# Performance work log

Measured on AMD Instinct MI355X. Metric: run time of the kernel, lower is better.

Reference implementation:

```python
import jax, jax.numpy as jnp
import numpy as np

N_VERTS = 100000
N_FACES = 200000
C = 512


def setup_inputs() -> dict:
    key = jax.random.key(0)
    ks = jax.random.split(key, 12)
    x = jax.random.normal(ks[0], (1, N_VERTS, C), dtype=jnp.float32) * 0.1
    verts = jax.random.normal(ks[1], (N_VERTS, 3), dtype=jnp.float32)
    faces = jax.random.randint(ks[2], (N_FACES, 3), 0, N_VERTS, dtype=jnp.int32)
    def lin(k, fan_in, fan_out):
        return jax.random.normal(k, (fan_in, fan_out), dtype=jnp.float32) / np.sqrt(fan_in)
    return {
        "x": x, "verts": verts, "faces": faces,
        "W1": lin(ks[3], C, C),    "b1": jnp.zeros((C,), jnp.float32),
        "W2": lin(ks[4], C, 512),  "b2": jnp.zeros((512,), jnp.float32),
        "W3": lin(ks[5], 512, 256),"b3": jnp.zeros((256,), jnp.float32),
        "W4": lin(ks[6], 256, 12), "b4": jnp.zeros((12,), jnp.float32),
    }


def special_procrustes(M):
    # roma.special_procrustes: nearest rotation in SO(3) to M, batched [F,3,3]
    U, S, Vh = jnp.linalg.svd(M)
    det = jnp.linalg.det(jnp.matmul(U, Vh))  # [F]
    D = jnp.stack([jnp.ones_like(det), jnp.ones_like(det), det], axis=-1)  # [F,3]
    return jnp.matmul(U * D[:, None, :], Vh)


def reference(x, verts, faces, W1, b1, W2, b2, W3, b3, W4, b4):
    N = verts.shape[0]
    F = faces.shape[0]
    # prism base: gather 3 vertex positions per face -> [F,3,3]
    prism_base = verts[faces]
    # gather features of the 3 face vertices and mean over them -> [F,C]
    feat = x[0][faces].mean(axis=1)
    # mlp_refine
    h = jax.nn.relu(feat @ W1 + b1)
    h = jax.nn.relu(h @ W2 + b2)
    h = jax.nn.relu(h @ W3 + b3)
    out = h @ W4 + b4  # [F,12]
    # batched 3x3 Procrustes rotation + translation
    rotations = special_procrustes(out[:, :9].reshape(F, 3, 3))
    translations = out[:, 9:]  # [F,3]
    transformed_prism = jnp.matmul(prism_base, rotations) + translations[:, None, :]  # [F,3,3]
    # scatter-add back to vertices with per-vertex face-count normalization
    flat_idx = faces.reshape(-1)  # [3F]
    summed = jax.ops.segment_sum(transformed_prism.reshape(-1, 3), flat_idx, num_segments=N)
    counts = jax.ops.segment_sum(jnp.ones((3 * F,), jnp.float32), flat_idx, num_segments=N)
    features = summed / jnp.clip(counts, 1.0)[:, None]  # [N,3]
    return features[None], transformed_prism, rotations
```

## Files before the change

### kernel.cpp

```cpp
#include <hip/hip_runtime.h>
#include <stdint.h>

typedef __attribute__((ext_vector_type(8))) short short8;
typedef __attribute__((ext_vector_type(4))) float f32x4;
typedef __attribute__((ext_vector_type(4))) unsigned short u16x4;

__device__ __forceinline__ unsigned short f2bf(float x) {
    union { float f; uint32_t u; } v; v.f = x;
    uint32_t u = v.u;
    uint32_t r = (u + 0x7FFFu + ((u >> 16) & 1u)) >> 16;
    return (unsigned short)r;
}
__device__ __forceinline__ float bf2f(unsigned short h) {
    union { uint32_t u; float f; } v; v.u = ((uint32_t)h) << 16;
    return v.f;
}

__device__ __forceinline__ void gld_lds16(const void* g, void* s) {
    __builtin_amdgcn_global_load_lds(
        (const __attribute__((address_space(1))) void*)(uintptr_t)g,
        (__attribute__((address_space(3))) void*)(uint32_t)(uintptr_t)s,
        16, 0, 0);
}

__device__ __forceinline__ f32x4 mfma16(short8 a, short8 b, f32x4 c) {
    return __builtin_amdgcn_mfma_f32_16x16x32_bf16(a, b, c, 0, 0, 0);
}

__global__ void zero_kernel(float* __restrict__ sums, float* __restrict__ counts, int nverts) {
    int t = blockIdx.x * 256 + threadIdx.x;
    if (t < nverts * 3) sums[t] = 0.0f;
    if (t < nverts)     counts[t] = 0.0f;
}

__global__ void prep_weights(const float* __restrict__ W1, const float* __restrict__ W2,
                             const float* __restrict__ W3,
                             unsigned short* __restrict__ w1h, unsigned short* __restrict__ w1l,
                             unsigned short* __restrict__ w2h, unsigned short* __restrict__ w2l,
                             unsigned short* __restrict__ w3h, unsigned short* __restrict__ w3l) {
    int t = blockIdx.x * 256 + threadIdx.x;
    float v; unsigned short *ph, *pl; size_t o;
    if (t < 262144) {
        int k = t >> 9, n = t & 511;
        v = W1[t]; o = (size_t)n * 512 + k; ph = w1h; pl = w1l;
    } else if (t < 524288) {
        int u = t - 262144; int k = u >> 9, n = u & 511;
        v = W2[u]; o = (size_t)n * 512 + k; ph = w2h; pl = w2l;
    } else if (t < 655360) {
        int u = t - 524288; int k = u >> 8, n = u & 255;
        v = W3[u]; o = (size_t)n * 512 + k; ph = w3h; pl = w3l;
    } else return;
    unsigned short hi = f2bf(v);
    unsigned short lo = f2bf(v - bf2f(hi));
    ph[o] = hi; pl[o] = lo;
}

__global__ void gather_relu(const float* __restrict__ y, const int* __restrict__ faces,
                            const float* __restrict__ b1,
                            unsigned short* __restrict__ Hh, unsigned short* __restrict__ Hl,
                            int nfaces, int mrows) {
    int t = blockIdx.x * 256 + threadIdx.x;
    if (t >= (mrows << 7)) return;
    int r = t >> 7;
    int c = (t & 127) << 2;
    f32x4 m = {0.f, 0.f, 0.f, 0.f};
    if (r < nfaces) {
        int i0 = faces[3 * r], i1 = faces[3 * r + 1], i2 = faces[3 * r + 2];
        f32x4 a = *(const f32x4*)(y + (size_t)i0 * 512 + c);
        f32x4 b = *(const f32x4*)(y + (size_t)i1 * 512 + c);
        f32x4 d = *(const f32x4*)(y + (size_t)i2 * 512 + c);
        m = (a + b + d) * (1.0f / 3.0f);
    }
    f32x4 bv = *(const f32x4*)(b1 + c);
    u16x4 hv, lv;
#pragma unroll
    for (int j = 0; j < 4; ++j) {
        float h = fmaxf(m[j] + bv[j], 0.0f);
        unsigned short hi = f2bf(h);
        hv[j] = hi;
        lv[j] = f2bf(h - bf2f(hi));
    }
    *(u16x4*)(Hh + (size_t)r * 512 + c) = hv;
    *(u16x4*)(Hl + (size_t)r * 512 + c) = lv;
}

__global__ void gather_mean(const float* __restrict__ x, const int* __restrict__ faces,
                            unsigned short* __restrict__ Fhi, unsigned short* __restrict__ Flo,
                            int fbase, int fcount, int mrows) {
    int t = blockIdx.x * 256 + threadIdx.x;
    if (t >= (mrows << 7)) return;
    int r = t >> 7;
    int c = (t & 127) << 2;
    f32x4 m = {0.f, 0.f, 0.f, 0.f};
    if (r < fcount) {
        int f = fbase + r;
        int i0 = faces[3 * f], i1 = faces[3 * f + 1], i2 = faces[3 * f + 2];
        f32x4 a = *(const f32x4*)(x + (size_t)i0 * 512 + c);
        f32x4 b = *(const f32x4*)(x + (size_t)i1 * 512 + c);
        f32x4 d = *(const f32x4*)(x + (size_t)i2 * 512 + c);
        m = (a + b + d) * (1.0f / 3.0f);
    }
    u16x4 hv, lv;
#pragma unroll
    for (int j = 0; j < 4; ++j) {
        unsigned short hi = f2bf(m[j]);
        hv[j] = hi;
        lv[j] = f2bf(m[j] - bf2f(hi));
    }
    *(u16x4*)(Fhi + (size_t)r * 512 + c) = hv;
    *(u16x4*)(Flo + (size_t)r * 512 + c) = lv;
}

template<int OUT>
__global__ __launch_bounds__(256, 2)
void gemm_pipe(const unsigned short* __restrict__ Ahi, const unsigned short* __restrict__ Alo,
               const unsigned short* __restrict__ Bhi, const unsigned short* __restrict__ Blo,
               const float* __restrict__ bias,
               void* __restrict__ Out0, unsigned short* __restrict__ Olo,
               int N, int K, int nt) {
    __shared__ __align__(16) unsigned short sm[2][4][128 * 32];

    const int tid  = threadIdx.x;
    const int lane = tid & 63;
    const int w    = tid >> 6;
    const int wr = w >> 1, wc = w & 1;

    const int nwg  = gridDim.x;
    const int orig = blockIdx.x;
    const int q = nwg >> 3, r8 = nwg & 7;
    const int xcd = orig & 7, idx = orig >> 3;
    const int wg = (xcd < r8 ? xcd * (q + 1) : r8 * (q + 1) + (xcd - r8) * q) + idx;
    const int m0 = (wg / nt) << 7;
    const int n0 = (wg % nt) << 7;

    f32x4 acc[4][4] = {};

    const int s_lo  = w * 64 + lane;
    const int row0  = s_lo >> 2;
    const int c0    = ((s_lo & 3) - ((row0 >> 1) & 3)) & 3;
    const int s_hi  = 256 + s_lo;
    const int row1  = (s_hi >> 2) & 127;
    const int c1    = ((s_hi & 3) - ((row1 >> 1) & 3)) & 3;

    auto stage = [&](int b, int t) {
        const int k0 = t << 5;
        const unsigned short* const mats[4] = {Ahi, Alo, Bhi, Blo};
#pragma unroll
        for (int p = 0; p < 4; ++p) {
            const unsigned short* mat = mats[p];
            const int base0 = (p < 2) ? m0 : n0;
            gld_lds16(mat + (size_t)(base0 + row0) * K + (k0 + (c0 << 3)),
                      &sm[b][p][(w * 64) * 8]);
            gld_lds16(mat + (size_t)(base0 + row1) * K + (k0 + (c1 << 3)),
                      &sm[b][p][(256 + w * 64) * 8]);
        }
    };

    const int NT = K >> 5;
    stage(0, 0);
    stage(1, 1);

    const int kc  = lane >> 4;
    const int rbA = (wr << 6) + (lane & 15);
    const int rbB = (wc << 6) + (lane & 15);

    for (int t = 0; t < NT; ++t) {
        const int cur = t & 1;

        if (t + 1 < NT) asm volatile("s_waitcnt vmcnt(8)" ::: "memory");
        else            asm volatile("s_waitcnt vmcnt(0)" ::: "memory");
        __builtin_amdgcn_s_barrier();

        short8 ah[4], al[4], bh[4], bl[4];
#pragma unroll
        for (int m = 0; m < 4; ++m) {
            const int r   = rbA + (m << 4);
            const int off = r * 32 + (((kc + (r >> 1)) & 3) << 3);
            ah[m] = *(const short8*)&sm[cur][0][off];
            al[m] = *(const short8*)&sm[cur][1][off];
        }
#pragma unroll
        for (int n = 0; n < 4; ++n) {
            const int r   = rbB + (n << 4);
            const int off = r * 32 + (((kc + (r >> 1)) & 3) << 3);
            bh[n] = *(const short8*)&sm[cur][2][off];
            bl[n] = *(const short8*)&sm[cur][3][off];
        }
        asm volatile("s_waitcnt lgkmcnt(0)" ::: "memory");
        __builtin_amdgcn_sched_barrier(0);
        __builtin_amdgcn_s_barrier();

        if (t + 2 < NT) stage(cur, t + 2);

        __builtin_amdgcn_s_setprio(1);
#pragma unroll
        for (int m = 0; m < 4; ++m)
#pragma unroll
            for (int n = 0; n < 4; ++n)
                acc[m][n] = mfma16(ah[m], bh[n], acc[m][n]);
#pragma unroll
        for (int m = 0; m < 4; ++m)
#pragma unroll
            for (int n = 0; n < 4; ++n)
                acc[m][n] = mfma16(al[m], bh[n], acc[m][n]);
#pragma unroll
        for (int m = 0; m < 4; ++m)
#pragma unroll
            for (int n = 0; n < 4; ++n)
                acc[m][n] = mfma16(ah[m], bl[n], acc[m][n]);
        __builtin_amdgcn_s_setprio(0);
    }

#pragma unroll
    for (int n = 0; n < 4; ++n) {
        const int col = n0 + (wc << 6) + (n << 4) + (lane & 15);
        const float bv = (OUT == 1) ? 0.0f : bias[col];
#pragma unroll
        for (int m = 0; m < 4; ++m) {
            const int rbase = m0 + (wr << 6) + (m << 4) + ((lane >> 4) << 2);
#pragma unroll
            for (int j = 0; j < 4; ++j) {
                const size_t o = (size_t)(rbase + j) * N + col;
                if (OUT == 1) {
                    ((float*)Out0)[o] = acc[m][n][j];
                } else if (OUT == 2) {
                    ((float*)Out0)[o] = fmaxf(acc[m][n][j] + bv, 0.0f);
                } else {
                    float v = fmaxf(acc[m][n][j] + bv, 0.0f);
                    unsigned short hi = f2bf(v);
                    ((unsigned short*)Out0)[o] = hi;
                    Olo[o] = f2bf(v - bf2f(hi));
                }
            }
        }
    }
}

__global__ __launch_bounds__(256, 2)
void gemm_l1(const float* __restrict__ X,
             const unsigned short* __restrict__ Bhi, const unsigned short* __restrict__ Blo,
             float* __restrict__ Out,
             int N, int K, int nt, int nvalid) {
    __shared__ __align__(16) unsigned short sm[2][4][128 * 32];

    const int tid  = threadIdx.x;
    const int lane = tid & 63;
    const int w    = tid >> 6;
    const int wr = w >> 1, wc = w & 1;

    const int nwg  = gridDim.x;
    const int orig = blockIdx.x;
    const int q = nwg >> 3, r8 = nwg & 7;
    const int xcd = orig & 7, idx = orig >> 3;
    const int wg = (xcd < r8 ? xcd * (q + 1) : r8 * (q + 1) + (xcd - r8) * q) + idx;
    const int m0 = (wg / nt) << 7;
    const int n0 = (wg % nt) << 7;

    f32x4 acc[4][4] = {};

    int arow[2], achk[2], adst[2], avalid[2];
#pragma unroll
    for (int i = 0; i < 2; ++i) {
        const int s   = i * 256 + tid;
        const int row = s >> 2;
        const int c   = s & 3;
        arow[i]   = row;
        achk[i]   = c;
        adst[i]   = row * 32 + (((c + (row >> 1)) & 3) << 3);
        avalid[i] = (m0 + row) < nvalid;
    }
    const int s_lo  = w * 64 + lane;
    const int row0  = s_lo >> 2;
    const int c0    = ((s_lo & 3) - ((row0 >> 1) & 3)) & 3;
    const int s_hi  = 256 + s_lo;
    const int row1  = (s_hi >> 2) & 127;
    const int c1    = ((s_hi & 3) - ((row1 >> 1) & 3)) & 3;

    f32x4 fA[2][2];

    auto issueA = [&](int t) {
        const int k0 = t << 5;
#pragma unroll
        for (int i = 0; i < 2; ++i) {
            const int gr = avalid[i] ? (m0 + arow[i]) : 0;
            const float* src = X + (size_t)gr * K + (k0 + (achk[i] << 3));
            fA[i][0] = *(const f32x4*)src;
            fA[i][1] = *(const f32x4*)(src + 4);
        }
    };
    auto issueB = [&](int b, int t) {
        const int k0 = t << 5;
        gld_lds16(Bhi + (size_t)(n0 + row0) * K + (k0 + (c0 << 3)), &sm[b][2][(w * 64) * 8]);
        gld_lds16(Bhi + (size_t)(n0 + row1) * K + (k0 + (c1 << 3)), &sm[b][2][(256 + w * 64) * 8]);
        gld_lds16(Blo + (size_t)(n0 + row0) * K + (k0 + (c0 << 3)), &sm[b][3][(w * 64) * 8]);
        gld_lds16(Blo + (size_t)(n0 + row1) * K + (k0 + (c1 << 3)), &sm[b][3][(256 + w * 64) * 8]);
    };
    auto cvtWriteA = [&](int b) {
#pragma unroll
        for (int i = 0; i < 2; ++i) {
            short8 hv, lv;
#pragma unroll
            for (int j = 0; j < 8; ++j) {
                float f = avalid[i] ? fA[i][j >> 2][j & 3] : 0.0f;
                unsigned short hi = f2bf(f);
                hv[j] = (short)hi;
                lv[j] = (short)f2bf(f - bf2f(hi));
            }
            *(short8*)&sm[b][0][adst[i]] = hv;
            *(short8*)&sm[b][1][adst[i]] = lv;
        }
    };

    const int NT = K >> 5;
    issueA(0); issueB(0, 0);
    asm volatile("s_waitcnt vmcnt(4)" ::: "memory");
    cvtWriteA(0);
    issueA(1); issueB(1, 1);
    asm volatile("s_waitcnt vmcnt(4)" ::: "memory");
    cvtWriteA(1);
    asm volatile("s_waitcnt lgkmcnt(0)" ::: "memory");

    const int kc  = lane >> 4;
    const int rbA = (wr << 6) + (lane & 15);
    const int rbB = (wc << 6) + (lane & 15);

    for (int t = 0; t < NT; ++t) {
        const int cur = t & 1;

        if (t + 1 < NT) asm volatile("s_waitcnt vmcnt(4)" ::: "memory");
        else            asm volatile("s_waitcnt vmcnt(0)" ::: "memory");
        __builtin_amdgcn_s_barrier();

        short8 ah[4], al[4], bh[4], bl[4];
#pragma unroll
        for (int m = 0; m < 4; ++m) {
            const int r   = rbA + (m << 4);
            const int off = r * 32 + (((kc + (r >> 1)) & 3) << 3);
            ah[m] = *(const short8*)&sm[cur][0][off];
            al[m] = *(const short8*)&sm[cur][1][off];
        }
#pragma unroll
        for (int n = 0; n < 4; ++n) {
            const int r   = rbB + (n << 4);
            const int off = r * 32 + (((kc + (r >> 1)) & 3) << 3);
            bh[n] = *(const short8*)&sm[cur][2][off];
            bl[n] = *(const short8*)&sm[cur][3][off];
        }
        asm volatile("s_waitcnt lgkmcnt(0)" ::: "memory");
        __builtin_amdgcn_sched_barrier(0);
        __builtin_amdgcn_s_barrier();

        const int doStage = (t + 2 < NT);
        if (doStage) { issueA(t + 2); issueB(cur, t + 2); }

        __builtin_amdgcn_s_setprio(1);
#pragma unroll
        for (int m = 0; m < 4; ++m)
#pragma unroll
            for (int n = 0; n < 4; ++n)
                acc[m][n] = mfma16(ah[m], bh[n], acc[m][n]);
#pragma unroll
        for (int m = 0; m < 4; ++m)
#pragma unroll
            for (int n = 0; n < 4; ++n)
                acc[m][n] = mfma16(al[m], bh[n], acc[m][n]);
#pragma unroll
        for (int m = 0; m < 4; ++m)
#pragma unroll
            for (int n = 0; n < 4; ++n)
                acc[m][n] = mfma16(ah[m], bl[n], acc[m][n]);
        __builtin_amdgcn_s_setprio(0);

        if (doStage) {
            asm volatile("s_waitcnt vmcnt(4)" ::: "memory");
            cvtWriteA(cur);
        }
    }

#pragma unroll
    for (int n = 0; n < 4; ++n) {
        const int col = n0 + (wc << 6) + (n << 4) + (lane & 15);
#pragma unroll
        for (int m = 0; m < 4; ++m) {
            const int rbase = m0 + (wr << 6) + (m << 4) + ((lane >> 4) << 2);
#pragma unroll
            for (int j = 0; j < 4; ++j)
                Out[(size_t)(rbase + j) * N + col] = acc[m][n][j];
        }
    }
}

#define JROT(app, aqq, apq, apz, aqz, vp0, vp1, vp2, vq0, vq1, vq2) do {          \
    float _apq = (apq);                                                            \
    if (fabsf(_apq) > 1e-30f) {                                                    \
        float _tau = ((aqq) - (app)) / (2.0f * _apq);                              \
        float _t = copysignf(1.0f, _tau) / (fabsf(_tau) + sqrtf(1.0f + _tau*_tau));\
        float _c = 1.0f / sqrtf(1.0f + _t*_t);                                     \
        float _s = _t * _c;                                                        \
        (app) = (app) - _t * _apq;                                                 \
        (aqq) = (aqq) + _t * _apq;                                                 \
        (apq) = 0.0f;                                                              \
        float _pz = (apz), _qz = (aqz);                                            \
        (apz) = _c * _pz - _s * _qz;                                               \
        (aqz) = _s * _pz + _c * _qz;                                               \
        float _x;                                                                  \
        _x = (vp0); (vp0) = _c*_x - _s*(vq0); (vq0) = _s*_x + _c*(vq0);            \
        _x = (vp1); (vp1) = _c*_x - _s*(vq1); (vq1) = _s*_x + _c*(vq1);            \
        _x = (vp2); (vp2) = _c*_x - _s*(vq2); (vq2) = _s*_x + _c*(vq2);            \
    }                                                                              \
} while (0)

#define SWAP3(la, lb, x0, y0, z0, x1, y1, z1) do {                \
    float _tm;                                                    \
    _tm = la; la = lb; lb = _tm;                                  \
    _tm = x0; x0 = x1; x1 = _tm;                                  \
    _tm = y0; y0 = y1; y1 = _tm;                                  \
    _tm = z0; z0 = z1; z1 = _tm;                                  \
} while (0)

__global__ void face_kernel(const float* __restrict__ H3,
                            const float* __restrict__ W4, const float* __restrict__ b4,
                            const float* __restrict__ verts, const int* __restrict__ faces,
                            float* __restrict__ out_tp, float* __restrict__ out_rot,
                            float* __restrict__ sums, float* __restrict__ counts,
                            int fbase, int fcount) {
    __shared__ float sW[256 * 12 + 12];
    for (int i = threadIdx.x; i < 256 * 12 + 12; i += 256)
        sW[i] = (i < 256 * 12) ? W4[i] : b4[i - 256 * 12];
    __syncthreads();

    const int r = blockIdx.x * 256 + threadIdx.x;
    if (r >= fcount) return;
    const int f = fbase + r;

    float o[12];
#pragma unroll
    for (int n = 0; n < 12; ++n) o[n] = sW[3072 + n];
    const f32x4* ph = (const f32x4*)(H3 + (size_t)r * 256);
    for (int kb = 0; kb < 64; ++kb) {
        f32x4 hv = ph[kb];
#pragma unroll
        for (int kk = 0; kk < 4; ++kk) {
            float val = hv[kk];
            const float* wrow = &sW[(kb * 4 + kk) * 12];
#pragma unroll
            for (int n = 0; n < 12; ++n) o[n] = fmaf(val, wrow[n], o[n]);
        }
    }

    const float M00=o[0], M01=o[1], M02=o[2];
    const float M10=o[3], M11=o[4], M12=o[5];
    const float M20=o[6], M21=o[7], M22=o[8];
    const float t0 =o[9], t1 =o[10], t2 =o[11];

    float a00 = M00*M00 + M10*M10 + M20*M20;
    float a11 = M01*M01 + M11*M11 + M21*M21;
    float a22 = M02*M02 + M12*M12 + M22*M22;
    float a01 = M00*M01 + M10*M11 + M20*M21;
    float a02 = M00*M02 + M10*M12 + M20*M22;
    float a12 = M01*M02 + M11*M12 + M21*M22;

    float v00=1.f, v01=0.f, v02=0.f;
    float v10=0.f, v11=1.f, v12=0.f;
    float v20=0.f, v21=0.f, v22=1.f;
#pragma unroll
    for (int sweep = 0; sweep < 5; ++sweep) {
        JROT(a00, a11, a01, a02, a12, v00, v10, v20, v01, v11, v21);
        JROT(a00, a22, a02, a01, a12, v00, v10, v20, v02, v12, v22);
        JROT(a11, a22, a12, a01, a02, v01, v11, v21, v02, v12, v22);
    }
    float l0 = a00, l1 = a11, l2 = a22;
    if (l0 < l1) SWAP3(l0, l1, v00, v10, v20, v01, v11, v21);
    if (l0 < l2) SWAP3(l0, l2, v00, v10, v20, v02, v12, v22);
    if (l1 < l2) SWAP3(l1, l2, v01, v11, v21, v02, v12, v22);

    float b1x = M00*v00 + M01*v10 + M02*v20;
    float b1y = M10*v00 + M11*v10 + M12*v20;
    float b1z = M20*v00 + M21*v10 + M22*v20;
    float b2x = M00*v01 + M01*v11 + M02*v21;
    float b2y = M10*v01 + M11*v11 + M12*v21;
    float b2z = M20*v01 + M21*v11 + M22*v21;

    float n1 = sqrtf(b1x*b1x + b1y*b1y + b1z*b1z);
    float u1x, u1y, u1z;
    if (n1 > 1e-25f) { float in = 1.0f / n1; u1x = b1x*in; u1y = b1y*in; u1z = b1z*in; }
    else             { u1x = 1.f; u1y = 0.f; u1z = 0.f; }

    float dp  = b2x*u1x + b2y*u1y + b2z*u1z;
    float w2x = b2x - dp*u1x, w2y = b2y - dp*u1y, w2z = b2z - dp*u1z;
    float n2  = sqrtf(w2x*w2x + w2y*w2y + w2z*w2z);
    float u2x, u2y, u2z;
    if (n2 > 1e-25f) { float in = 1.0f / n2; u2x = w2x*in; u2y = w2y*in; u2z = w2z*in; }
    else {
        float ex = (fabsf(u1x) < 0.9f) ? 1.f : 0.f;
        float ey = 1.f - ex;
        float cx = -u1z * ey, cy = u1z * ex, cz = u1x * ey - u1y * ex;
        float cn = rsqrtf(cx*cx + cy*cy + cz*cz);
        u2x = cx * cn; u2y = cy * cn; u2z = cz * cn;
    }
    float u3x = u1y*u2z - u1z*u2y;
    float u3y = u1z*u2x - u1x*u2z;
    float u3z = u1x*u2y - u1y*u2x;

    float dv = v00*(v11*v22 - v12*v21) - v01*(v10*v22 - v12*v20) + v02*(v10*v21 - v11*v20);
    if (dv < 0.f) { v02 = -v02; v12 = -v12; v22 = -v22; }

    float R00 = u1x*v00 + u2x*v01 + u3x*v02;
    float R01 = u1x*v10 + u2x*v11 + u3x*v12;
    float R02 = u1x*v20 + u2x*v21 + u3x*v22;
    float R10 = u1y*v00 + u2y*v01 + u3y*v02;
    float R11 = u1y*v10 + u2y*v11 + u3y*v12;
    float R12 = u1y*v20 + u2y*v21 + u3y*v22;
    float R20 = u1z*v00 + u2z*v01 + u3z*v02;
    float R21 = u1z*v10 + u2z*v11 + u3z*v12;
    float R22 = u1z*v20 + u2z*v21 + u3z*v22;

    float* rp = out_rot + (size_t)f * 9;
    rp[0]=R00; rp[1]=R01; rp[2]=R02;
    rp[3]=R10; rp[4]=R11; rp[5]=R12;
    rp[6]=R20; rp[7]=R21; rp[8]=R22;

    float* tp = out_tp + (size_t)f * 9;
    const int idx[3] = { faces[3*f], faces[3*f+1], faces[3*f+2] };
#pragma unroll
    for (int j = 0; j < 3; ++j) {
        const int vi = idx[j];
        float px = verts[3*vi], py = verts[3*vi+1], pz = verts[3*vi+2];
        float q0 = px*R00 + py*R10 + pz*R20 + t0;
        float q1 = px*R01 + py*R11 + pz*R21 + t1;
        float q2 = px*R02 + py*R12 + pz*R22 + t2;
        tp[j*3+0] = q0; tp[j*3+1] = q1; tp[j*3+2] = q2;
        atomicAdd(&sums[(size_t)vi*3+0], q0);
        atomicAdd(&sums[(size_t)vi*3+1], q1);
        atomicAdd(&sums[(size_t)vi*3+2], q2);
        atomicAdd(&counts[vi], 1.0f);
    }
}

__global__ void finalize_kernel(float* __restrict__ feats, const float* __restrict__ counts, int nverts) {
    int v = blockIdx.x * 256 + threadIdx.x;
    if (v >= nverts) return;
    float c = fmaxf(counts[v], 1.0f);
    feats[v*3+0] = feats[v*3+0] / c;
    feats[v*3+1] = feats[v*3+1] / c;
    feats[v*3+2] = feats[v*3+2] / c;
}

extern "C" void kernel_launch(void* const* d_in, const int* in_sizes, int n_in,
                              void* d_out, int out_size, void* d_ws, size_t ws_size,
                              hipStream_t stream) {
    const float* x     = (const float*)d_in[0];
    const float* verts = (const float*)d_in[1];
    const int*   faces = (const int*)d_in[2];
    const float* W1 = (const float*)d_in[3];
    const float* b1 = (const float*)d_in[4];
    const float* W2 = (const float*)d_in[5];
    const float* b2 = (const float*)d_in[6];
    const float* W3 = (const float*)d_in[7];
    const float* b3 = (const float*)d_in[8];
    const float* W4 = (const float*)d_in[9];
    const float* b4 = (const float*)d_in[10];

    const int nverts = in_sizes[1] / 3;
    const int nfaces = in_sizes[2] / 3;

    float* out_feats = (float*)d_out;
    float* out_tp    = out_feats + (size_t)nverts * 3;
    float* out_rot   = out_tp + (size_t)nfaces * 9;

    char* ws = (char*)d_ws;
    size_t cur = 0;
    auto carve = [&](size_t bytes) -> void* {
        void* p = ws + cur;
        cur += (bytes + 255) & ~(size_t)255;
        return p;
    };
    unsigned short* w1h = (unsigned short*)carve(512 * 512 * 2);
    unsigned short* w1l = (unsigned short*)carve(512 * 512 * 2);
    unsigned short* w2h = (unsigned short*)carve(512 * 512 * 2);
    unsigned short* w2l = (unsigned short*)carve(512 * 512 * 2);
    unsigned short* w3h = (unsigned short*)carve(256 * 512 * 2);
    unsigned short* w3l = (unsigned short*)carve(256 * 512 * 2);
    float* counts = (float*)carve((size_t)nverts * 4);

    const long MV = ((long)nverts + 127) & ~127L;
    const long MF = ((long)nfaces + 127) & ~127L;
    const size_t szY   = (size_t)MV * 512 * 4;
    const size_t szH1  = (size_t)MF * 512 * 2;
    const size_t szH3f = (size_t)MF * 256 * 4;

    const size_t sR1 = (szY > szH1) ? szY : szH1;
    const size_t sR2 = (szH1 > szH3f) ? szH1 : szH3f;
    const size_t sR3 = szH1;
    const size_t sR4 = szH1;
    const size_t need = cur + sR1 + sR2 + sR3 + sR4 + 4 * 256;

    zero_kernel<<<(nverts * 3 + 255) / 256, 256, 0, stream>>>(out_feats, counts, nverts);
    prep_weights<<<(655360 + 255) / 256, 256, 0, stream>>>(W1, W2, W3, w1h, w1l, w2h, w2l, w3h, w3l);

    if (ws_size >= need) {
        char* R1 = (char*)carve(sR1);
        char* R2 = (char*)carve(sR2);
        char* R3 = (char*)carve(sR3);
        char* R4 = (char*)carve(sR4);
        float*          y   = (float*)R1;
        unsigned short* h2h = (unsigned short*)R1;
        unsigned short* h1h = (unsigned short*)R2;
        float*          h3  = (float*)R2;
        unsigned short* h1l = (unsigned short*)R3;
        unsigned short* h2l = (unsigned short*)R4;

        gemm_l1<<<(int)(MV / 128) * 4, 256, 0, stream>>>(x, w1h, w1l, y, 512, 512, 4, nverts);

        gather_relu<<<(int)(MF * 128 / 256), 256, 0, stream>>>(y, faces, b1, h1h, h1l, nfaces, (int)MF);

        gemm_pipe<0><<<(int)(MF / 128) * 4, 256, 0, stream>>>(h1h, h1l, w2h, w2l, b2, h2h, h2l, 512, 512, 4);
        gemm_pipe<2><<<(int)(MF / 128) * 2, 256, 0, stream>>>(h2h, h2l, w3h, w3l, b3, h3, nullptr, 256, 512, 2);

        face_kernel<<<(nfaces + 255) / 256, 256, 0, stream>>>(h3, W4, b4, verts, faces,
                                                              out_tp, out_rot, out_feats, counts,
                                                              0, nfaces);
    } else {
        long mpad = MF;
        size_t avail = (ws_size > cur) ? (ws_size - cur) : 0;
        long chp = (long)(avail / 4096);
        chp &= ~127L;
        if (chp > mpad) chp = mpad;
        if (chp < 128) chp = 128;
        unsigned short* bAh = (unsigned short*)carve((size_t)chp * 512 * 2);
        unsigned short* bAl = (unsigned short*)carve((size_t)chp * 512 * 2);
        unsigned short* bBh = (unsigned short*)carve((size_t)chp * 512 * 2);
        unsigned short* bBl = (unsigned short*)carve((size_t)chp * 512 * 2);

        for (long base = 0; base < nfaces; base += chp) {
            long rem = (long)nfaces - base;
            int cnt = (int)((rem < chp) ? rem : chp);
            int mc  = (cnt + 127) & ~127;

            gather_mean<<<mc / 2, 256, 0, stream>>>(x, faces, bAh, bAl, (int)base, cnt, mc);
            gemm_pipe<0><<<(mc / 128) * 4, 256, 0, stream>>>(bAh, bAl, w1h, w1l, b1, bBh, bBl, 512, 512, 4);
            gemm_pipe<0><<<(mc / 128) * 4, 256, 0, stream>>>(bBh, bBl, w2h, w2l, b2, bAh, bAl, 512, 512, 4);
            gemm_pipe<2><<<(mc / 128) * 2, 256, 0, stream>>>(bAh, bAl, w3h, w3l, b3, (float*)bBh, nullptr, 256, 512, 2);
            face_kernel<<<(cnt + 255) / 256, 256, 0, stream>>>((float*)bBh, W4, b4, verts, faces,
                                                               out_tp, out_rot, out_feats, counts,
                                                               (int)base, cnt);
        }
    }

    finalize_kernel<<<(nverts + 255) / 256, 256, 0, stream>>>(out_feats, counts, nverts);
}
```

Before: 1.430 ms.

## Fuse face gather, mean, bias and ReLU into layer-2 GEMM A-operand loading

```diff
diff --git a/kernel.cpp b/kernel.cpp
--- a/kernel.cpp
+++ b/kernel.cpp
@@ -55,35 +55,6 @@
     ph[o] = hi; pl[o] = lo;
 }
 
-__global__ void gather_relu(const float* __restrict__ y, const int* __restrict__ faces,
-                            const float* __restrict__ b1,
-                            unsigned short* __restrict__ Hh, unsigned short* __restrict__ Hl,
-                            int nfaces, int mrows) {
-    int t = blockIdx.x * 256 + threadIdx.x;
-    if (t >= (mrows << 7)) return;
-    int r = t >> 7;
-    int c = (t & 127) << 2;
-    f32x4 m = {0.f, 0.f, 0.f, 0.f};
-    if (r < nfaces) {
-        int i0 = faces[3 * r], i1 = faces[3 * r + 1], i2 = faces[3 * r + 2];
-        f32x4 a = *(const f32x4*)(y + (size_t)i0 * 512 + c);
-        f32x4 b = *(const f32x4*)(y + (size_t)i1 * 512 + c);
-        f32x4 d = *(const f32x4*)(y + (size_t)i2 * 512 + c);
-        m = (a + b + d) * (1.0f / 3.0f);
-    }
-    f32x4 bv = *(const f32x4*)(b1 + c);
-    u16x4 hv, lv;
-#pragma unroll
-    for (int j = 0; j < 4; ++j) {
-        float h = fmaxf(m[j] + bv[j], 0.0f);
-        unsigned short hi = f2bf(h);
-        hv[j] = hi;
-        lv[j] = f2bf(h - bf2f(hi));
-    }
-    *(u16x4*)(Hh + (size_t)r * 512 + c) = hv;
-    *(u16x4*)(Hl + (size_t)r * 512 + c) = lv;
-}
-
 __global__ void gather_mean(const float* __restrict__ x, const int* __restrict__ faces,
                             unsigned short* __restrict__ Fhi, unsigned short* __restrict__ Flo,
                             int fbase, int fcount, int mrows) {
@@ -386,6 +357,185 @@
 #pragma unroll
             for (int j = 0; j < 4; ++j)
                 Out[(size_t)(rbase + j) * N + col] = acc[m][n][j];
+        }
+    }
+}
+
+__global__ __launch_bounds__(256, 2)
+void gemm_l2g(const float* __restrict__ Y, const int* __restrict__ faces,
+              const float* __restrict__ b1,
+              const unsigned short* __restrict__ Bhi, const unsigned short* __restrict__ Blo,
+              const float* __restrict__ bias2,
+              unsigned short* __restrict__ Ohi, unsigned short* __restrict__ Olo,
+              int N, int K, int nt, int nvalid) {
+    __shared__ __align__(16) unsigned short sm[2][4][128 * 32];
+
+    const int tid  = threadIdx.x;
+    const int lane = tid & 63;
+    const int w    = tid >> 6;
+    const int wr = w >> 1, wc = w & 1;
+
+    const int nwg  = gridDim.x;
+    const int orig = blockIdx.x;
+    const int q = nwg >> 3, r8 = nwg & 7;
+    const int xcd = orig & 7, idx = orig >> 3;
+    const int wg = (xcd < r8 ? xcd * (q + 1) : r8 * (q + 1) + (xcd - r8) * q) + idx;
+    const int m0 = (wg / nt) << 7;
+    const int n0 = (wg % nt) << 7;
+
+    f32x4 acc[4][4] = {};
+
+    int achk[2], adst[2], avalid[2];
+    int fidx[2][3];
+#pragma unroll
+    for (int i = 0; i < 2; ++i) {
+        const int s   = i * 256 + tid;
+        const int row = s >> 2;
+        const int c   = s & 3;
+        achk[i]   = c;
+        adst[i]   = row * 32 + (((c + (row >> 1)) & 3) << 3);
+        const int gf  = m0 + row;
+        avalid[i] = gf < nvalid;
+        const int gfs = avalid[i] ? gf : 0;
+        fidx[i][0] = faces[3 * gfs];
+        fidx[i][1] = faces[3 * gfs + 1];
+        fidx[i][2] = faces[3 * gfs + 2];
+    }
+    const int s_lo  = w * 64 + lane;
+    const int row0  = s_lo >> 2;
+    const int c0    = ((s_lo & 3) - ((row0 >> 1) & 3)) & 3;
+    const int s_hi  = 256 + s_lo;
+    const int row1  = (s_hi >> 2) & 127;
+    const int c1    = ((s_hi & 3) - ((row1 >> 1) & 3)) & 3;
+
+    f32x4 fA[2][3][2];
+    f32x4 fb[2][2];
+
+    auto issueA = [&](int t) {
+        const int k0 = t << 5;
+#pragma unroll
+        for (int i = 0; i < 2; ++i) {
+            const int koff = k0 + (achk[i] << 3);
+#pragma unroll
+            for (int r = 0; r < 3; ++r) {
+                const float* src = Y + (size_t)fidx[i][r] * K + koff;
+                fA[i][r][0] = *(const f32x4*)src;
+                fA[i][r][1] = *(const f32x4*)(src + 4);
+            }
+            fb[i][0] = *(const f32x4*)(b1 + koff);
+            fb[i][1] = *(const f32x4*)(b1 + koff + 4);
+        }
+    };
+    auto issueB = [&](int b, int t) {
+        const int k0 = t << 5;
+        gld_lds16(Bhi + (size_t)(n0 + row0) * K + (k0 + (c0 << 3)), &sm[b][2][(w * 64) * 8]);
+        gld_lds16(Bhi + (size_t)(n0 + row1) * K + (k0 + (c1 << 3)), &sm[b][2][(256 + w * 64) * 8]);
+        gld_lds16(Blo + (size_t)(n0 + row0) * K + (k0 + (c0 << 3)), &sm[b][3][(w * 64) * 8]);
+        gld_lds16(Blo + (size_t)(n0 + row1) * K + (k0 + (c1 << 3)), &sm[b][3][(256 + w * 64) * 8]);
+    };
+    auto cvtWriteA = [&](int b) {
+        const float third = 1.0f / 3.0f;
+#pragma unroll
+        for (int i = 0; i < 2; ++i) {
+            short8 hv, lv;
+#pragma unroll
+            for (int j = 0; j < 8; ++j) {
+                const int h = j >> 2, e = j & 3;
+                float f = 0.0f;
+                if (avalid[i]) {
+                    f = (fA[i][0][h][e] + fA[i][1][h][e] + fA[i][2][h][e]) * third + fb[i][h][e];
+                    f = fmaxf(f, 0.0f);
+                }
+                unsigned short hi = f2bf(f);
+                hv[j] = (short)hi;
+                lv[j] = (short)f2bf(f - bf2f(hi));
+            }
+            *(short8*)&sm[b][0][adst[i]] = hv;
+            *(short8*)&sm[b][1][adst[i]] = lv;
+        }
+    };
+
+    const int NT = K >> 5;
+    issueA(0); issueB(0, 0);
+    asm volatile("s_waitcnt vmcnt(4)" ::: "memory");
+    cvtWriteA(0);
+    issueA(1); issueB(1, 1);
+    asm volatile("s_waitcnt vmcnt(4)" ::: "memory");
+    cvtWriteA(1);
+    asm volatile("s_waitcnt lgkmcnt(0)" ::: "memory");
+
+    const int kc  = lane >> 4;
+    const int rbA = (wr << 6) + (lane & 15);
+    const int rbB = (wc << 6) + (lane & 15);
+
+    for (int t = 0; t < NT; ++t) {
+        const int cur = t & 1;
+
+        if (t + 1 < NT) asm volatile("s_waitcnt vmcnt(4)" ::: "memory");
+        else            asm volatile("s_waitcnt vmcnt(0)" ::: "memory");
+        __builtin_amdgcn_s_barrier();
+
+        short8 ah[4], al[4], bh[4], bl[4];
+#pragma unroll
+        for (int m = 0; m < 4; ++m) {
+            const int r   = rbA + (m << 4);
+            const int off = r * 32 + (((kc + (r >> 1)) & 3) << 3);
+            ah[m] = *(const short8*)&sm[cur][0][off];
+            al[m] = *(const short8*)&sm[cur][1][off];
+        }
+#pragma unroll
+        for (int n = 0; n < 4; ++n) {
+            const int r   = rbB + (n << 4);
+            const int off = r * 32 + (((kc + (r >> 1)) & 3) << 3);
+            bh[n] = *(const short8*)&sm[cur][2][off];
+            bl[n] = *(const short8*)&sm[cur][3][off];
+        }
+        asm volatile("s_waitcnt lgkmcnt(0)" ::: "memory");
+        __builtin_amdgcn_sched_barrier(0);
+        __builtin_amdgcn_s_barrier();
+
+        const int doStage = (t + 2 < NT);
+        if (doStage) { issueA(t + 2); issueB(cur, t + 2); }
+
+        __builtin_amdgcn_s_setprio(1);
+#pragma unroll
+        for (int m = 0; m < 4; ++m)
+#pragma unroll
+            for (int n = 0; n < 4; ++n)
+                acc[m][n] = mfma16(ah[m], bh[n], acc[m][n]);
+#pragma unroll
+        for (int m = 0; m < 4; ++m)
+#pragma unroll
+            for (int n = 0; n < 4; ++n)
+                acc[m][n] = mfma16(al[m], bh[n], acc[m][n]);
+#pragma unroll
+        for (int m = 0; m < 4; ++m)
+#pragma unroll
+            for (int n = 0; n < 4; ++n)
+                acc[m][n] = mfma16(ah[m], bl[n], acc[m][n]);
+        __builtin_amdgcn_s_setprio(0);
+
+        if (doStage) {
+            asm volatile("s_waitcnt vmcnt(4)" ::: "memory");
+            cvtWriteA(cur);
+        }
+    }
+
+#pragma unroll
+    for (int n = 0; n < 4; ++n) {
+        const int col = n0 + (wc << 6) + (n << 4) + (lane & 15);
+        const float bv = bias2[col];
+#pragma unroll
+        for (int m = 0; m < 4; ++m) {
+            const int rbase = m0 + (wr << 6) + (m << 4) + ((lane >> 4) << 2);
+#pragma unroll
+            for (int j = 0; j < 4; ++j) {
+                const size_t o = (size_t)(rbase + j) * N + col;
+                float v = fmaxf(acc[m][n][j] + bv, 0.0f);
+                unsigned short hi = f2bf(v);
+                Ohi[o] = hi;
+                Olo[o] = f2bf(v - bf2f(hi));
+            }
         }
     }
 }
@@ -586,14 +736,14 @@
     const long MV = ((long)nverts + 127) & ~127L;
     const long MF = ((long)nfaces + 127) & ~127L;
     const size_t szY   = (size_t)MV * 512 * 4;
-    const size_t szH1  = (size_t)MF * 512 * 2;
+    const size_t szH2  = (size_t)MF * 256 * 2;
+    const size_t szH2w = (size_t)MF * 512 * 2;
     const size_t szH3f = (size_t)MF * 256 * 4;
 
-    const size_t sR1 = (szY > szH1) ? szY : szH1;
-    const size_t sR2 = (szH1 > szH3f) ? szH1 : szH3f;
-    const size_t sR3 = szH1;
-    const size_t sR4 = szH1;
-    const size_t need = cur + sR1 + sR2 + sR3 + sR4 + 4 * 256;
+    const size_t sR1 = (szY > szH3f) ? szY : szH3f;
+    const size_t sR2 = szH2w;
+    const size_t sR3 = szH2w;
+    const size_t need = cur + sR1 + sR2 + sR3 + 4 * 256;
 
     zero_kernel<<<(nverts * 3 + 255) / 256, 256, 0, stream>>>(out_feats, counts, nverts);
     prep_weights<<<(655360 + 255) / 256, 256, 0, stream>>>(W1, W2, W3, w1h, w1l, w2h, w2l, w3h, w3l);
@@ -602,19 +752,16 @@
         char* R1 = (char*)carve(sR1);
         char* R2 = (char*)carve(sR2);
         char* R3 = (char*)carve(sR3);
-        char* R4 = (char*)carve(sR4);
         float*          y   = (float*)R1;
-        unsigned short* h2h = (unsigned short*)R1;
-        unsigned short* h1h = (unsigned short*)R2;
-        float*          h3  = (float*)R2;
-        unsigned short* h1l = (unsigned short*)R3;
-        unsigned short* h2l = (unsigned short*)R4;
+        float*          h3  = (float*)R1;
+        unsigned short* h2h = (unsigned short*)R2;
+        unsigned short* h2l = (unsigned short*)R3;
 
         gemm_l1<<<(int)(MV / 128) * 4, 256, 0, stream>>>(x, w1h, w1l, y, 512, 512, 4, nverts);
 
-        gather_relu<<<(int)(MF * 128 / 256), 256, 0, stream>>>(y, faces, b1, h1h, h1l, nfaces, (int)MF);
-
-        gemm_pipe<0><<<(int)(MF / 128) * 4, 256, 0, stream>>>(h1h, h1l, w2h, w2l, b2, h2h, h2l, 512, 512, 4);
+        gemm_l2g<<<(int)(MF / 128) * 4, 256, 0, stream>>>(y, faces, b1, w2h, w2l, b2,
+                                                          h2h, h2l, 512, 512, 4, nfaces);
+
         gemm_pipe<2><<<(int)(MF / 128) * 2, 256, 0, stream>>>(h2h, h2l, w3h, w3l, b3, h3, nullptr, 256, 512, 2);
 
         face_kernel<<<(nfaces + 255) / 256, 256, 0, stream>>>(h3, W4, b4, verts, faces,
```

After: 1.240 ms. -13.3%, faster.
